# Performance work log

Hardware: AMD Instinct MI355X
Metric: run time of the kernel (lower is better)

Reference implementation:

```python
import jax, jax.numpy as jnp
import numpy as np

HIDDEN = 1024
HEADS = 16
MEM = 2
D_H = HIDDEN // HEADS
NEG = -1.0e9


def setup_inputs() -> dict:
    key = jax.random.key(0)
    ks = jax.random.split(key, 8)
    B, M, N = 16, 512, 512
    s = 1.0 / np.sqrt(HIDDEN)
    return {
        "x": jax.random.normal(ks[0], (B, M, HIDDEN), dtype=jnp.float32),
        "y": jax.random.normal(ks[1], (B, N, HIDDEN), dtype=jnp.float32),
        "mask_x": jax.random.randint(ks[2], (B, M), 0, 2, dtype=jnp.int64),
        "mask_y": jax.random.randint(ks[3], (B, N), 0, 2, dtype=jnp.int64),
        "Wx": jax.random.normal(ks[4], (HIDDEN, HIDDEN), dtype=jnp.float32) * s,
        "Wy": jax.random.normal(ks[5], (HIDDEN, HIDDEN), dtype=jnp.float32) * s,
        "x_memory": jax.random.normal(ks[6], (MEM, HIDDEN), dtype=jnp.float32),
        "y_memory": jax.random.normal(ks[7], (MEM, HIDDEN), dtype=jnp.float32),
    }


def _project(t, mem, W):
    # prepend memory tokens, then linear (torch Linear: t @ W^T), split heads
    B = t.shape[0]
    t_mem = jnp.concatenate([jnp.broadcast_to(mem[None], (B, MEM, HIDDEN)), t], axis=1)
    proj = t_mem @ W.T
    proj = proj.reshape(B, t_mem.shape[1], HEADS, D_H)
    return t_mem, proj


def reference(x, y, mask_x, mask_y, Wx, Wy, x_memory, y_memory):
    B = x.shape[0]
    mem_mask = jnp.ones((B, MEM), dtype=mask_x.dtype)
    mx = jnp.concatenate([mem_mask, mask_x], axis=1)  # [B, M+MEM]
    my = jnp.concatenate([mem_mask, mask_y], axis=1)  # [B, N+MEM]

    X_mem, X_proj = _project(x, x_memory, Wx)  # [B,Mm,H], [B,Mm,heads,d_h]
    Y_mem, Y_proj = _project(y, y_memory, Wy)

    # affinity: [B, heads, Mm, Nm]
    aff = jnp.einsum("bmhd,bnhd->bhmn", X_proj, Y_proj)
    aff = jnp.where(mx[:, None, :, None] == 0, NEG, aff)
    aff = jnp.where(my[:, None, None, :] == 0, NEG, aff)

    attn_X = jnp.mean(jax.nn.softmax(aff, axis=2), axis=1)  # [B, Mm, Nm]
    attn_Y = jnp.mean(jax.nn.softmax(aff, axis=3), axis=1)  # [B, Mm, Nm]

    X_in_Y = jnp.einsum("bmn,bmh->bnh", attn_X, X_mem)[:, MEM:, :]  # [B, N, H]
    Y_in_X = jnp.einsum("bmn,bnh->bmh", attn_Y, Y_mem)[:, MEM:, :]  # [B, M, H]
    return X_in_Y, Y_in_X
```

## Files before the change

### kernel.cpp

```cpp
#include <hip/hip_runtime.h>

#define B_   16
#define SEQ  512
#define MM   514
#define HID  1024
#define NH   16
#define DH   64
#define KP   544
#define MTOT (B_ * MM)
#define UNI  (1.0f/514.0f)

typedef unsigned short us;
typedef __attribute__((ext_vector_type(4))) float f32x4;
typedef __attribute__((ext_vector_type(8))) short short8;
typedef __attribute__((ext_vector_type(8))) _Float16 half8;

__device__ __forceinline__ us f2bf(float f) {
  unsigned int u = __float_as_uint(f);
  u = (u + 0x7FFFu + ((u >> 16) & 1u)) >> 16;
  return (us)u;
}
__device__ __forceinline__ float bf2f(us h) {
  return __uint_as_float(((unsigned int)h) << 16);
}
__device__ __forceinline__ us f2h(float f) {
  _Float16 h = (_Float16)f;
  return *(us*)&h;
}
__device__ __forceinline__ unsigned cvt_pk_bf16(float lo, float hi) {
  unsigned d;
  asm("v_cvt_pk_bf16_f32 %0, %1, %2" : "=v"(d) : "v"(lo), "v"(hi));
  return d;
}
__device__ __forceinline__ uint4 pack8_pk(f32x4 v0, f32x4 v1) {
  uint4 r;
  r.x = cvt_pk_bf16(v0[0], v0[1]);
  r.y = cvt_pk_bf16(v0[2], v0[3]);
  r.z = cvt_pk_bf16(v1[0], v1[1]);
  r.w = cvt_pk_bf16(v1[2], v1[3]);
  return r;
}

__global__ __launch_bounds__(256) void proj_fused(
    const float* __restrict__ x, const float* __restrict__ y,
    const float* __restrict__ xm, const float* __restrict__ ym,
    const float* __restrict__ Wx, const float* __restrict__ Wy,
    us* __restrict__ Px, us* __restrict__ Py) {
  const int nt = blockIdx.x, mt = blockIdx.y, which = blockIdx.z;
  const float* tin  = which ? y  : x;
  const float* mvec = which ? ym : xm;
  const float* W    = which ? Wy : Wx;
  us* P             = which ? Py : Px;
  __shared__ __align__(16) us As[128 * 40];
  __shared__ __align__(16) us Bs[128 * 40];
  const int tid = threadIdx.x;
  const int lane = tid & 63, wave = tid >> 6;
  const int c = lane & 15, q = lane >> 4;
  const int wr = wave >> 1, wc = wave & 1;

  const int srow = tid >> 1, sch = (tid & 1) * 16;
  const int grow = mt * 128 + srow;
  const float* asrc = nullptr;
  if (grow < MTOT) {
    const int gb = grow / MM, gt = grow - gb * MM;
    asrc = (gt < 2) ? (mvec + (size_t)gt * HID + sch)
                    : (tin + ((size_t)(gb * SEQ + gt - 2)) * HID + sch);
  }
  const float* bsrc = W + ((size_t)(nt * 128 + srow)) * HID + sch;
  us* wAp = &As[srow * 40 + sch];
  us* wBp = &Bs[srow * 40 + sch];
  const us* rA = &As[(wr * 64 + c) * 40 + q * 8];
  const us* rB = &Bs[(wc * 64 + c) * 40 + q * 8];

  f32x4 acc[4][4];
#pragma unroll
  for (int i = 0; i < 4; i++)
#pragma unroll
    for (int j = 0; j < 4; j++) acc[i][j] = (f32x4){0.f, 0.f, 0.f, 0.f};

  f32x4 pa[4], pb[4];
#pragma unroll
  for (int u = 0; u < 4; u++) pa[u] = (f32x4){0.f, 0.f, 0.f, 0.f};
  if (asrc) {
#pragma unroll
    for (int u = 0; u < 4; u++) pa[u] = *(const f32x4*)(asrc + u * 4);
  }
#pragma unroll
  for (int u = 0; u < 4; u++) pb[u] = *(const f32x4*)(bsrc + u * 4);

  for (int kk = 0; kk < HID; kk += 32) {
    __syncthreads();
    *(uint4*)wAp       = pack8_pk(pa[0], pa[1]);
    *(uint4*)(wAp + 8) = pack8_pk(pa[2], pa[3]);
    *(uint4*)wBp       = pack8_pk(pb[0], pb[1]);
    *(uint4*)(wBp + 8) = pack8_pk(pb[2], pb[3]);
    __syncthreads();
    if (kk + 32 < HID) {
      if (asrc) {
#pragma unroll
        for (int u = 0; u < 4; u++) pa[u] = *(const f32x4*)(asrc + kk + 32 + u * 4);
      }
#pragma unroll
      for (int u = 0; u < 4; u++) pb[u] = *(const f32x4*)(bsrc + kk + 32 + u * 4);
    }
    short8 a[4], bb[4];
#pragma unroll
    for (int i = 0; i < 4; i++) a[i] = *(const short8*)(rA + i * 16 * 40);
#pragma unroll
    for (int j = 0; j < 4; j++) bb[j] = *(const short8*)(rB + j * 16 * 40);
#pragma unroll
    for (int i = 0; i < 4; i++)
#pragma unroll
      for (int j = 0; j < 4; j++)
        acc[i][j] = __builtin_amdgcn_mfma_f32_16x16x32_bf16(a[i], bb[j], acc[i][j], 0, 0, 0);
  }
#pragma unroll
  for (int i = 0; i < 4; i++) {
#pragma unroll
    for (int r = 0; r < 4; r++) {
      int gr = mt * 128 + wr * 64 + i * 16 + q * 4 + r;
      if (gr < MTOT) {
        size_t rb = (size_t)gr * HID;
#pragma unroll
        for (int j = 0; j < 4; j++)
          P[rb + nt * 128 + wc * 64 + j * 16 + c] = f2bf(acc[i][j][r]);
      }
    }
  }
}

__device__ __forceinline__ void stage_bf(
    us* Xs, const us* P, int b, int r0, int h, int tid) {
#pragma unroll
  for (int i = 0; i < 2; i++) {
    int idx = tid + i * 256;
    int row = idx >> 3, qq = idx & 7;
    *(uint4*)&Xs[row * 72 + qq * 8] =
        *(const uint4*)(P + ((size_t)(b * MM + min(r0 + row, MM - 1))) * HID + h * DH + qq * 8);
  }
}

__global__ __launch_bounds__(512) void sums_big(
    const us* __restrict__ Px, const us* __restrict__ Py,
    const int* __restrict__ mx, const int* __restrict__ my,
    float* __restrict__ Sums) {
  const int half = blockIdx.x, h = blockIdx.y, b = blockIdx.z;
  const int NCH = half ? 5 : 4;
  const int n0 = half * 256;
  __shared__ __align__(16) us Ys[320 * 72];
  __shared__ __align__(16) us Xs[64 * 72];
  __shared__ float cS[320];
  __shared__ int myS[320];
  __shared__ int mxS[576];
  const int tid = threadIdx.x;
  const int lane = tid & 63, wave = tid >> 6;
  const int c = lane & 15, q = lane >> 4;
  const int strip = wave & 3, cgrp = wave >> 2;
  const int chm = (NCH + 1) >> 1;
  const int ch0 = cgrp ? chm : 0;
  const int ch1 = cgrp ? NCH : chm;

  for (int i = tid; i < 320; i += 512) {
    cS[i] = 0.f;
    int n = n0 + i;
    myS[i] = (n >= MM) ? 0 : ((n < 2) ? 1 : my[b * SEQ + n - 2]);
  }
  for (int i = tid; i < 576; i += 512)
    mxS[i] = (i >= MM) ? 0 : ((i < 2) ? 1 : mx[b * SEQ + i - 2]);
  {
    const int row8 = tid >> 3, qq = tid & 7;
    for (int it = 0; it < NCH; it++) {
      int row = it * 64 + row8;
      int grow = min(n0 + row, MM - 1);
      *(uint4*)&Ys[row * 72 + qq * 8] =
          *(const uint4*)(Py + ((size_t)(b * MM + grow)) * HID + h * DH + qq * 8);
    }
  }
  __syncthreads();

  const size_t base = ((size_t)(b * NH + h)) * MM;
  const size_t COLOFF = (size_t)B_ * NH * MM;

  for (int mt = 0; mt < 9; mt++) {
    {
      const int row8 = tid >> 3, qq = tid & 7;
      int grow = min(mt * 64 + row8, MM - 1);
      *(uint4*)&Xs[row8 * 72 + qq * 8] =
          *(const uint4*)(Px + ((size_t)(b * MM + grow)) * HID + h * DH + qq * 8);
    }
    __syncthreads();
    short8 a0 = *(const short8*)&Xs[(strip * 16 + c) * 72 + q * 8];
    short8 a1 = *(const short8*)&Xs[(strip * 16 + c) * 72 + q * 8 + 32];
    int rm[4];
#pragma unroll
    for (int r = 0; r < 4; r++) rm[r] = mxS[mt * 64 + strip * 16 + q * 4 + r];
    float rowp[4] = {0.f, 0.f, 0.f, 0.f};
    for (int ch = ch0; ch < ch1; ch++) {
#pragma unroll
      for (int ss = 0; ss < 4; ss++) {
        int nloc = ch * 64 + ss * 16 + c;
        short8 b0 = *(const short8*)&Ys[nloc * 72 + q * 8];
        short8 b1 = *(const short8*)&Ys[nloc * 72 + q * 8 + 32];
        f32x4 av = (f32x4){0.f, 0.f, 0.f, 0.f};
        av = __builtin_amdgcn_mfma_f32_16x16x32_bf16(a0, b0, av, 0, 0, 0);
        av = __builtin_amdgcn_mfma_f32_16x16x32_bf16(a1, b1, av, 0, 0, 0);
        int cmv = myS[nloc];
        float colp = 0.f;
#pragma unroll
        for (int r = 0; r < 4; r++) {
          float e = (rm[r] && cmv) ? __expf(av[r]) : 0.f;
          rowp[r] += e;
          colp += e;
        }
        colp += __shfl_xor(colp, 16);
        colp += __shfl_xor(colp, 32);
        if (q == 0) atomicAdd(&cS[nloc], colp);
      }
    }
#pragma unroll
    for (int d = 1; d < 16; d <<= 1)
#pragma unroll
      for (int r = 0; r < 4; r++) rowp[r] += __shfl_xor(rowp[r], d, 16);
    if (c == 0) {
#pragma unroll
      for (int r = 0; r < 4; r++) {
        int m = mt * 64 + strip * 16 + q * 4 + r;
        if (m < MM) atomicAdd(&Sums[base + m], rowp[r]);
      }
    }
    __syncthreads();
  }
  for (int i = tid; i < NCH * 64; i += 512) {
    int n = n0 + i;
    if (n < MM) Sums[COLOFF + base + n] = cS[i];
  }
}

__global__ __launch_bounds__(256) void inv_kernel(float* __restrict__ Sums) {
  int i = blockIdx.x * 256 + threadIdx.x;
  if (i < 2 * B_ * NH * MM) {
    float s = Sums[i];
    Sums[i] = (s > 0.f) ? (1.f / s) : -1.f;
  }
}

__global__ __launch_bounds__(256) void attn_mfma2(
    const us* __restrict__ Px, const us* __restrict__ Py,
    const int* __restrict__ mx, const int* __restrict__ my,
    const float* __restrict__ Inv,
    us* __restrict__ attnXT, us* __restrict__ attnY) {
  const int nt = blockIdx.x, mt = blockIdx.y, b = blockIdx.z;
  __shared__ __align__(16) us Xs[64 * 72];
  __shared__ __align__(16) us Ys[64 * 72];
  const int tid = threadIdx.x;
  const int lane = tid & 63, wave = tid >> 6;
  const int c = lane & 15, q = lane >> 4;
  const size_t COLOFF = (size_t)B_ * NH * MM;

  int mreg[4], rm[4], ncol[4], cm[4];
#pragma unroll
  for (int r = 0; r < 4; r++) {
    mreg[r] = mt * 64 + wave * 16 + q * 4 + r;
    rm[r] = (mreg[r] >= MM) ? 0 : ((mreg[r] < 2) ? 1 : mx[b * SEQ + mreg[r] - 2]);
  }
#pragma unroll
  for (int s = 0; s < 4; s++) {
    ncol[s] = nt * 64 + s * 16 + c;
    cm[s] = (ncol[s] >= MM) ? 0 : ((ncol[s] < 2) ? 1 : my[b * SEQ + ncol[s] - 2]);
  }

  float aX[4][4], aY[4][4];
#pragma unroll
  for (int s = 0; s < 4; s++)
#pragma unroll
    for (int r = 0; r < 4; r++) { aX[s][r] = 0.f; aY[s][r] = 0.f; }

  for (int h = 0; h < NH; h++) {
    __syncthreads();
    stage_bf(Xs, Px, b, mt * 64, h, tid);
    stage_bf(Ys, Py, b, nt * 64, h, tid);
    __syncthreads();
    short8 a0 = *(const short8*)&Xs[(wave * 16 + c) * 72 + q * 8];
    short8 a1 = *(const short8*)&Xs[(wave * 16 + c) * 72 + q * 8 + 32];
    const size_t base = ((size_t)(b * NH + h)) * MM;
    float invR[4];
#pragma unroll
    for (int r = 0; r < 4; r++) invR[r] = Inv[base + min(mreg[r], MM - 1)];
#pragma unroll
    for (int s = 0; s < 4; s++) {
      float invC = Inv[COLOFF + base + min(ncol[s], MM - 1)];
      short8 b0 = *(const short8*)&Ys[(s * 16 + c) * 72 + q * 8];
      short8 b1 = *(const short8*)&Ys[(s * 16 + c) * 72 + q * 8 + 32];
      f32x4 av = (f32x4){0.f, 0.f, 0.f, 0.f};
      av = __builtin_amdgcn_mfma_f32_16x16x32_bf16(a0, b0, av, 0, 0, 0);
      av = __builtin_amdgcn_mfma_f32_16x16x32_bf16(a1, b1, av, 0, 0, 0);
#pragma unroll
      for (int r = 0; r < 4; r++) {
        float e = (rm[r] && cm[s]) ? __expf(av[r]) : 0.f;
        aY[s][r] += (invR[r] < 0.f) ? UNI : e * invR[r];
        aX[s][r] += (invC < 0.f) ? UNI : e * invC;
      }
    }
  }
#pragma unroll
  for (int s = 0; s < 4; s++) {
    if (ncol[s] < MM) {
      us* xrow = attnXT + ((size_t)(b * MM + ncol[s])) * KP;
      if (mreg[3] < MM) {
        uint2 w;
        w.x = (unsigned)f2h(aX[s][0] * 0.0625f) | ((unsigned)f2h(aX[s][1] * 0.0625f) << 16);
        w.y = (unsigned)f2h(aX[s][2] * 0.0625f) | ((unsigned)f2h(aX[s][3] * 0.0625f) << 16);
        *(uint2*)&xrow[mreg[0]] = w;
      } else {
#pragma unroll
        for (int r = 0; r < 4; r++)
          if (mreg[r] < MM) xrow[mreg[r]] = f2h(aX[s][r] * 0.0625f);
      }
#pragma unroll
      for (int r = 0; r < 4; r++)
        if (mreg[r] < MM)
          attnY[((size_t)(b * MM + mreg[r])) * KP + ncol[s]] = f2h(aY[s][r] * 0.0625f);
    }
  }
}

__global__ __launch_bounds__(256) void transpose_fused(
    const float* __restrict__ x, const float* __restrict__ y,
    const float* __restrict__ xm, const float* __restrict__ ym,
    us* __restrict__ XTx, us* __restrict__ XTy) {
  const int kt = blockIdx.x, ot = blockIdx.y;
  const int b = blockIdx.z & 15, path = blockIdx.z >> 4;
  const float* tin  = path ? y  : x;
  const float* mvec = path ? ym : xm;
  us* XT            = path ? XTy : XTx;
  __shared__ __align__(16) us T[64 * 40];
  const int tid = threadIdx.x;
  {
    const int row = tid >> 3;
    const int col8 = (tid & 7) * 8;
    const int kg = kt * 32 + row;
    const float* src = (kg < 2) ? (mvec + (size_t)kg * HID + ot * 64 + col8)
                     : (kg < MM) ? (tin + ((size_t)(b * SEQ + kg - 2)) * HID + ot * 64 + col8)
                                 : nullptr;
    f32x4 v0 = (f32x4){0.f, 0.f, 0.f, 0.f};
    f32x4 v1 = (f32x4){0.f, 0.f, 0.f, 0.f};
    if (src) { v0 = *(const f32x4*)src; v1 = *(const f32x4*)(src + 4); }
#pragma unroll
    for (int j = 0; j < 4; j++) T[(col8 + j) * 40 + row] = f2h(v0[j]);
#pragma unroll
    for (int j = 0; j < 4; j++) T[(col8 + 4 + j) * 40 + row] = f2h(v1[j]);
  }
  __syncthreads();
  const int orow = tid >> 2, kc = (tid & 3) * 8;
  uint4 w = *(const uint4*)&T[orow * 40 + kc];
  *(uint4*)&XT[((size_t)(b * HID + ot * 64 + orow)) * KP + kt * 32 + kc] = w;
}

__global__ __launch_bounds__(256) void outg_fused(
    const us* __restrict__ A0, const us* __restrict__ A1,
    const us* __restrict__ XTx, const us* __restrict__ XTy,
    float* __restrict__ outp) {
  const int ot = blockIdx.x, rt = blockIdx.y;
  const int b = blockIdx.z & 15, path = blockIdx.z >> 4;
  const us* A  = path ? A1 : A0;
  const us* XT = path ? XTy : XTx;
  float* op = outp + (path ? (size_t)B_ * SEQ * HID : 0);
  const int r0 = rt * 128, o0 = ot * 128;
  __shared__ __align__(16) us As[128 * 40];
  __shared__ __align__(16) us Bs[128 * 40];
  const int tid = threadIdx.x;
  const int lane = tid & 63, wave = tid >> 6;
  const int c = lane & 15, q = lane >> 4;
  const int wr = wave >> 1, wc = wave & 1;

  const int srow = tid >> 2, sch = (tid & 3) * 8;
  const us* gA0 = A + ((size_t)(b * MM + 2 + r0 + srow)) * KP + sch;
  const us* gA1 = gA0 + (size_t)64 * KP;
  const us* gB0 = XT + ((size_t)(b * HID + o0 + srow)) * KP + sch;
  const us* gB1 = gB0 + (size_t)64 * KP;
  us* wA0 = &As[srow * 40 + sch];
  us* wA1 = wA0 + 64 * 40;
  us* wB0 = &Bs[srow * 40 + sch];
  us* wB1 = wB0 + 64 * 40;

  f32x4 acc[4][4];
#pragma unroll
  for (int i = 0; i < 4; i++)
#pragma unroll
    for (int j = 0; j < 4; j++) acc[i][j] = (f32x4){0.f, 0.f, 0.f, 0.f};

  const us* rA = &As[(wr * 64 + c) * 40 + q * 8];
  const us* rB = &Bs[(wc * 64 + c) * 40 + q * 8];

  uint4 pA0 = *(const uint4*)gA0;
  uint4 pA1 = *(const uint4*)gA1;
  uint4 pB0 = *(const uint4*)gB0;
  uint4 pB1 = *(const uint4*)gB1;

  for (int kk = 0; kk < KP; kk += 32) {
    __syncthreads();
    *(uint4*)wA0 = pA0;
    *(uint4*)wA1 = pA1;
    *(uint4*)wB0 = pB0;
    *(uint4*)wB1 = pB1;
    __syncthreads();
    if (kk + 32 < KP) {
      pA0 = *(const uint4*)(gA0 + kk + 32);
      pA1 = *(const uint4*)(gA1 + kk + 32);
      pB0 = *(const uint4*)(gB0 + kk + 32);
      pB1 = *(const uint4*)(gB1 + kk + 32);
    }
    half8 a[4], bb[4];
#pragma unroll
    for (int i = 0; i < 4; i++) a[i] = *(const half8*)(rA + i * 16 * 40);
#pragma unroll
    for (int j = 0; j < 4; j++) bb[j] = *(const half8*)(rB + j * 16 * 40);
#pragma unroll
    for (int i = 0; i < 4; i++)
#pragma unroll
      for (int j = 0; j < 4; j++)
        acc[i][j] = __builtin_amdgcn_mfma_f32_16x16x32_f16(a[i], bb[j], acc[i][j], 0, 0, 0);
  }
#pragma unroll
  for (int i = 0; i < 4; i++) {
#pragma unroll
    for (int rr = 0; rr < 4; rr++) {
      int r = r0 + wr * 64 + i * 16 + q * 4 + rr;
      size_t rowbase = ((size_t)(b * SEQ + r)) * HID;
#pragma unroll
      for (int j = 0; j < 4; j++)
        op[rowbase + o0 + wc * 64 + j * 16 + c] = acc[i][j][rr];
    }
  }
}

__global__ __launch_bounds__(256) void attn_mfma_old(
    const us* __restrict__ Px, const us* __restrict__ Py,
    const int* __restrict__ mx, const int* __restrict__ my,
    const float* __restrict__ Inv,
    us* __restrict__ attnX, us* __restrict__ attnY,
    const int doX, const int doY) {
  const int nt = blockIdx.x, mt = blockIdx.y, b = blockIdx.z;
  __shared__ __align__(16) us Xs[64 * 72];
  __shared__ __align__(16) us Ys[64 * 72];
  const int tid = threadIdx.x;
  const int lane = tid & 63, wave = tid >> 6;
  const int c = lane & 15, q = lane >> 4;
  const size_t COLOFF = (size_t)B_ * NH * MM;

  int mreg[4], rm[4], ncol[4], cm[4];
#pragma unroll
  for (int r = 0; r < 4; r++) {
    mreg[r] = mt * 64 + wave * 16 + q * 4 + r;
    rm[r] = (mreg[r] >= MM) ? 0 : ((mreg[r] < 2) ? 1 : mx[b * SEQ + mreg[r] - 2]);
  }
#pragma unroll
  for (int s = 0; s < 4; s++) {
    ncol[s] = nt * 64 + s * 16 + c;
    cm[s] = (ncol[s] >= MM) ? 0 : ((ncol[s] < 2) ? 1 : my[b * SEQ + ncol[s] - 2]);
  }

  float aX[4][4], aY[4][4];
#pragma unroll
  for (int s = 0; s < 4; s++)
#pragma unroll
    for (int r = 0; r < 4; r++) { aX[s][r] = 0.f; aY[s][r] = 0.f; }

  for (int h = 0; h < NH; h++) {
    __syncthreads();
    stage_bf(Xs, Px, b, mt * 64, h, tid);
    stage_bf(Ys, Py, b, nt * 64, h, tid);
    __syncthreads();
    short8 a0 = *(const short8*)&Xs[(wave * 16 + c) * 72 + q * 8];
    short8 a1 = *(const short8*)&Xs[(wave * 16 + c) * 72 + q * 8 + 32];
    const size_t base = ((size_t)(b * NH + h)) * MM;
    float invR[4];
#pragma unroll
    for (int r = 0; r < 4; r++) invR[r] = Inv[base + min(mreg[r], MM - 1)];
#pragma unroll
    for (int s = 0; s < 4; s++) {
      float invC = Inv[COLOFF + base + min(ncol[s], MM - 1)];
      short8 b0 = *(const short8*)&Ys[(s * 16 + c) * 72 + q * 8];
      short8 b1 = *(const short8*)&Ys[(s * 16 + c) * 72 + q * 8 + 32];
      f32x4 av = (f32x4){0.f, 0.f, 0.f, 0.f};
      av = __builtin_amdgcn_mfma_f32_16x16x32_bf16(a0, b0, av, 0, 0, 0);
      av = __builtin_amdgcn_mfma_f32_16x16x32_bf16(a1, b1, av, 0, 0, 0);
#pragma unroll
      for (int r = 0; r < 4; r++) {
        float e = (rm[r] && cm[s]) ? __expf(av[r]) : 0.f;
        aY[s][r] += (invR[r] < 0.f) ? UNI : e * invR[r];
        aX[s][r] += (invC < 0.f) ? UNI : e * invC;
      }
    }
  }
#pragma unroll
  for (int s = 0; s < 4; s++) {
#pragma unroll
    for (int r = 0; r < 4; r++) {
      if (mreg[r] < MM && ncol[s] < MM) {
        size_t idx = ((size_t)(b * MM + mreg[r])) * MM + ncol[s];
        if (doX) attnX[idx] = f2bf(aX[s][r] * 0.0625f);
        if (doY) attnY[idx] = f2bf(aY[s][r] * 0.0625f);
      }
    }
  }
}

__global__ __launch_bounds__(256) void outg_kernel(
    const us* __restrict__ attn, const float* __restrict__ tin,
    const float* __restrict__ mvec, float* __restrict__ outp, const int trans) {
  const int otile = blockIdx.x, rtile = blockIdx.y, b = blockIdx.z;
  __shared__ __align__(16) float Ss[32 * 132];
  __shared__ __align__(16) float Ms[32 * 132];
  const int tid = threadIdx.x;
  const int r0 = rtile * 128, o0 = otile * 128;

  float acc[8][8];
#pragma unroll
  for (int i = 0; i < 8; i++)
#pragma unroll
    for (int j = 0; j < 8; j++) acc[i][j] = 0.f;

  for (int kk = 0; kk < 544; kk += 32) {
    __syncthreads();
    if (trans) {
      int rq = (tid & 31) * 4;
      int kr = tid >> 5;
#pragma unroll
      for (int kb = 0; kb < 32; kb += 8) {
        int k = kr + kb;
        int kg = kk + k;
        if (kg < MM) {
          const us* src = attn + ((size_t)(b * MM + kg)) * MM + 2 + r0 + rq;
          Ss[k * 132 + rq + 0] = bf2f(src[0]);
          Ss[k * 132 + rq + 1] = bf2f(src[1]);
          Ss[k * 132 + rq + 2] = bf2f(src[2]);
          Ss[k * 132 + rq + 3] = bf2f(src[3]);
        } else {
          Ss[k * 132 + rq + 0] = 0.f;
          Ss[k * 132 + rq + 1] = 0.f;
          Ss[k * 132 + rq + 2] = 0.f;
          Ss[k * 132 + rq + 3] = 0.f;
        }
      }
    } else {
      int r = tid >> 1;
      int kh = (tid & 1) * 16;
      const us* src = attn + ((size_t)(b * MM + 2 + r0 + r)) * MM;
#pragma unroll
      for (int j = 0; j < 16; j++) {
        int k = kh + j;
        int kg = kk + k;
        Ss[k * 132 + r] = (kg < MM) ? bf2f(src[kg]) : 0.f;
      }
    }
    {
      int k = tid >> 3;
      int oq = (tid & 7) * 16;
      int kg = kk + k;
      const float* mr = (kg < 2) ? (mvec + (size_t)kg * HID)
                      : (kg < MM) ? (tin + ((size_t)(b * SEQ + kg - 2)) * HID)
                                  : nullptr;
#pragma unroll
      for (int qq = 0; qq < 4; qq++) {
        f32x4 v = (f32x4){0.f, 0.f, 0.f, 0.f};
        if (mr) v = *(const f32x4*)(mr + o0 + oq + qq * 4);
        *(f32x4*)&Ms[k * 132 + oq + qq * 4] = v;
      }
    }
    __syncthreads();
    const int ty = tid >> 4, tx = tid & 15;
    for (int k = 0; k < 32; k++) {
      f32x4 s0 = *(const f32x4*)&Ss[k * 132 + ty * 4];
      f32x4 s1 = *(const f32x4*)&Ss[k * 132 + 64 + ty * 4];
      f32x4 m0 = *(const f32x4*)&Ms[k * 132 + tx * 4];
      f32x4 m1 = *(const f32x4*)&Ms[k * 132 + 64 + tx * 4];
#pragma unroll
      for (int i = 0; i < 4; i++) {
#pragma unroll
        for (int j = 0; j < 4; j++) {
          acc[i][j]         += s0[i] * m0[j];
          acc[i][j + 4]     += s0[i] * m1[j];
          acc[i + 4][j]     += s1[i] * m0[j];
          acc[i + 4][j + 4] += s1[i] * m1[j];
        }
      }
    }
  }
  const int ty = tid >> 4, tx = tid & 15;
#pragma unroll
  for (int ri = 0; ri < 2; ri++) {
#pragma unroll
    for (int i = 0; i < 4; i++) {
      int r = r0 + ri * 64 + ty * 4 + i;
      size_t rowbase = ((size_t)(b * SEQ + r)) * HID;
#pragma unroll
      for (int oi = 0; oi < 2; oi++) {
        int o = o0 + oi * 64 + tx * 4;
        f32x4 v;
#pragma unroll
        for (int j = 0; j < 4; j++) v[j] = acc[ri * 4 + i][oi * 4 + j];
        *(f32x4*)&outp[rowbase + o] = v;
      }
    }
  }
}

extern "C" void kernel_launch(void* const* d_in, const int* in_sizes, int n_in,
                              void* d_out, int out_size, void* d_ws, size_t ws_size,
                              hipStream_t stream) {
  const float* x  = (const float*)d_in[0];
  const float* y  = (const float*)d_in[1];
  const int* mask_x = (const int*)d_in[2];
  const int* mask_y = (const int*)d_in[3];
  const float* Wx = (const float*)d_in[4];
  const float* Wy = (const float*)d_in[5];
  const float* xm = (const float*)d_in[6];
  const float* ym = (const float*)d_in[7];
  float* out = (float*)d_out;

  const size_t szSums = (size_t)2 * B_ * NH * MM * 4;
  const size_t szP    = (size_t)B_ * MM * HID * 2;
  const size_t szAtt  = (size_t)B_ * MM * MM * 2;
  const size_t szAttP = (size_t)B_ * MM * KP * 2;
  const size_t szXT   = (size_t)B_ * HID * KP * 2;
  const size_t R_off  = szSums + 2 * szAttP;
  const size_t needNew = R_off + 2 * szXT;

  char* ws = (char*)d_ws;

  if (ws_size >= needNew) {
    float* Sums = (float*)ws;
    us* A0  = (us*)(ws + szSums);
    us* A1  = (us*)(ws + szSums + szAttP);
    us* Px  = (us*)(ws + R_off);
    us* Py  = (us*)(ws + R_off + szP);
    us* XTx = (us*)(ws + R_off);
    us* XTy = (us*)(ws + R_off + szXT);

    proj_fused<<<dim3(8, 65, 2), 256, 0, stream>>>(x, y, xm, ym, Wx, Wy, Px, Py);
    hipMemsetAsync(Sums, 0, szSums, stream);
    hipMemsetAsync(A0, 0, 2 * szAttP, stream);
    sums_big<<<dim3(2, 16, 16), 512, 0, stream>>>(Px, Py, mask_x, mask_y, Sums);
    inv_kernel<<<dim3((2 * B_ * NH * MM + 255) / 256), 256, 0, stream>>>(Sums);
    attn_mfma2<<<dim3(9, 9, 16), 256, 0, stream>>>(Px, Py, mask_x, mask_y, Sums, A0, A1);
    transpose_fused<<<dim3(17, 16, 32), 256, 0, stream>>>(x, y, xm, ym, XTx, XTy);
    outg_fused<<<dim3(8, 4, 32), 256, 0, stream>>>(A0, A1, XTx, XTy, out);
    return;
  }

  const int dual = (ws_size >= szSums + 2 * szP + 2 * szAtt) ? 1 : 0;
  float* Sums = (float*)(ws);
  us* Px = (us*)(ws + szSums);
  us* Py = (us*)(ws + szSums + szP);
  us* A0 = (us*)(ws + szSums + 2 * szP);
  us* A1 = dual ? (us*)(ws + szSums + 2 * szP + szAtt) : A0;

  proj_fused<<<dim3(8, 65, 2), 256, 0, stream>>>(x, y, xm, ym, Wx, Wy, Px, Py);
  hipMemsetAsync(Sums, 0, szSums, stream);
  sums_big<<<dim3(2, 16, 16), 512, 0, stream>>>(Px, Py, mask_x, mask_y, Sums);
  inv_kernel<<<dim3((2 * B_ * NH * MM + 255) / 256), 256, 0, stream>>>(Sums);

  if (dual) {
    attn_mfma_old<<<dim3(9, 9, 16), 256, 0, stream>>>(Px, Py, mask_x, mask_y, Sums, A0, A1, 1, 1);
    outg_kernel<<<dim3(8, 4, 16), 256, 0, stream>>>(A0, x, xm, out, 1);
    outg_kernel<<<dim3(8, 4, 16), 256, 0, stream>>>(A1, y, ym, out + (size_t)B_ * SEQ * HID, 0);
  } else {
    attn_mfma_old<<<dim3(9, 9, 16), 256, 0, stream>>>(Px, Py, mask_x, mask_y, Sums, A0, A0, 1, 0);
    outg_kernel<<<dim3(8, 4, 16), 256, 0, stream>>>(A0, x, xm, out, 1);
    attn_mfma_old<<<dim3(9, 9, 16), 256, 0, stream>>>(Px, Py, mask_x, mask_y, Sums, A0, A0, 0, 1);
    outg_kernel<<<dim3(8, 4, 16), 256, 0, stream>>>(A0, y, ym, out + (size_t)B_ * SEQ * HID, 0);
  }
}
```

Before: 405.3 us.

## Pre-convert projection inputs and weights to bf16 in a separate pass

Adds a prepack kernel that converts x/y (with memory tokens prepended) and Wx/Wy from fp32 to bf16 once, storing them in the output buffer as scratch space. The projection GEMM then loads bf16 directly, halving its global load bytes and dropping repeated per-tile conversion of W, which was re-read by every M tile. It also remaps block indices so consecutive blocks share an M tile across N tiles for better L2 reuse. The cost is an extra kernel launch plus a full read/write pass over the inputs, and it relies on the output buffer being free until the final kernel.

```diff
diff --git a/kernel.cpp b/kernel.cpp
--- a/kernel.cpp
+++ b/kernel.cpp
@@ -32,25 +32,56 @@
   asm("v_cvt_pk_bf16_f32 %0, %1, %2" : "=v"(d) : "v"(lo), "v"(hi));
   return d;
 }
-__device__ __forceinline__ uint4 pack8_pk(f32x4 v0, f32x4 v1) {
-  uint4 r;
-  r.x = cvt_pk_bf16(v0[0], v0[1]);
-  r.y = cvt_pk_bf16(v0[2], v0[3]);
-  r.z = cvt_pk_bf16(v1[0], v1[1]);
-  r.w = cvt_pk_bf16(v1[2], v1[3]);
-  return r;
-}
-
-__global__ __launch_bounds__(256) void proj_fused(
+
+__global__ __launch_bounds__(256) void prepack(
     const float* __restrict__ x, const float* __restrict__ y,
     const float* __restrict__ xm, const float* __restrict__ ym,
     const float* __restrict__ Wx, const float* __restrict__ Wy,
+    us* __restrict__ Abf, us* __restrict__ Wbf) {
+  const int tid = threadIdx.x;
+  const int row = blockIdx.x * 4 + (tid >> 6);
+  const int path = blockIdx.y;
+  const int lane = tid & 63;
+  const float* src;
+  us* dst;
+  if (row < MTOT) {
+    const int gb = row / MM, gt = row - gb * MM;
+    const float* tin = path ? y : x;
+    const float* mv  = path ? ym : xm;
+    src = (gt < 2) ? (mv + (size_t)gt * HID)
+                   : (tin + ((size_t)(gb * SEQ + gt - 2)) * HID);
+    dst = Abf + ((size_t)(path * MTOT + row)) * HID;
+  } else {
+    const int o = row - MTOT;
+    src = (path ? Wy : Wx) + (size_t)o * HID;
+    dst = Wbf + ((size_t)(path * HID + o)) * HID;
+  }
+  const float* s = src + lane * 16;
+  f32x4 v0 = *(const f32x4*)(s);
+  f32x4 v1 = *(const f32x4*)(s + 4);
+  f32x4 v2 = *(const f32x4*)(s + 8);
+  f32x4 v3 = *(const f32x4*)(s + 12);
+  uint4 w0, w1;
+  w0.x = cvt_pk_bf16(v0[0], v0[1]);  w0.y = cvt_pk_bf16(v0[2], v0[3]);
+  w0.z = cvt_pk_bf16(v1[0], v1[1]);  w0.w = cvt_pk_bf16(v1[2], v1[3]);
+  w1.x = cvt_pk_bf16(v2[0], v2[1]);  w1.y = cvt_pk_bf16(v2[2], v2[3]);
+  w1.z = cvt_pk_bf16(v3[0], v3[1]);  w1.w = cvt_pk_bf16(v3[2], v3[3]);
+  *(uint4*)(dst + lane * 16)     = w0;
+  *(uint4*)(dst + lane * 16 + 8) = w1;
+}
+
+__global__ __launch_bounds__(256) void proj_fused2(
+    const us* __restrict__ Abf, const us* __restrict__ Wbf,
     us* __restrict__ Px, us* __restrict__ Py) {
-  const int nt = blockIdx.x, mt = blockIdx.y, which = blockIdx.z;
-  const float* tin  = which ? y  : x;
-  const float* mvec = which ? ym : xm;
-  const float* W    = which ? Wy : Wx;
-  us* P             = which ? Py : Px;
+  const int lin = blockIdx.x + 8 * (blockIdx.y + 65 * blockIdx.z);
+  const int work = (lin & 7) * 130 + (lin >> 3);
+  const int path = (work >= 520) ? 1 : 0;
+  const int wrem = work - path * 520;
+  const int mt = wrem >> 3, nt = wrem & 7;
+  us* P = path ? Py : Px;
+  const us* Ab = Abf + (size_t)path * MTOT * HID;
+  const us* Wb = Wbf + (size_t)path * HID * HID;
+
   __shared__ __align__(16) us As[128 * 40];
   __shared__ __align__(16) us Bs[128 * 40];
   const int tid = threadIdx.x;
@@ -60,13 +91,8 @@
 
   const int srow = tid >> 1, sch = (tid & 1) * 16;
   const int grow = mt * 128 + srow;
-  const float* asrc = nullptr;
-  if (grow < MTOT) {
-    const int gb = grow / MM, gt = grow - gb * MM;
-    asrc = (gt < 2) ? (mvec + (size_t)gt * HID + sch)
-                    : (tin + ((size_t)(gb * SEQ + gt - 2)) * HID + sch);
-  }
-  const float* bsrc = W + ((size_t)(nt * 128 + srow)) * HID + sch;
+  const us* asrc = (grow < MTOT) ? (Ab + (size_t)grow * HID + sch) : nullptr;
+  const us* bsrc = Wb + (size_t)(nt * 128 + srow) * HID + sch;
   us* wAp = &As[srow * 40 + sch];
   us* wBp = &Bs[srow * 40 + sch];
   const us* rA = &As[(wr * 64 + c) * 40 + q * 8];
@@ -78,30 +104,25 @@
 #pragma unroll
     for (int j = 0; j < 4; j++) acc[i][j] = (f32x4){0.f, 0.f, 0.f, 0.f};
 
-  f32x4 pa[4], pb[4];
-#pragma unroll
-  for (int u = 0; u < 4; u++) pa[u] = (f32x4){0.f, 0.f, 0.f, 0.f};
-  if (asrc) {
-#pragma unroll
-    for (int u = 0; u < 4; u++) pa[u] = *(const f32x4*)(asrc + u * 4);
-  }
-#pragma unroll
-  for (int u = 0; u < 4; u++) pb[u] = *(const f32x4*)(bsrc + u * 4);
+  uint4 z4 = {0u, 0u, 0u, 0u};
+  uint4 pa0 = z4, pa1 = z4, pb0, pb1;
+  if (asrc) { pa0 = *(const uint4*)asrc; pa1 = *(const uint4*)(asrc + 8); }
+  pb0 = *(const uint4*)bsrc; pb1 = *(const uint4*)(bsrc + 8);
 
   for (int kk = 0; kk < HID; kk += 32) {
     __syncthreads();
-    *(uint4*)wAp       = pack8_pk(pa[0], pa[1]);
-    *(uint4*)(wAp + 8) = pack8_pk(pa[2], pa[3]);
-    *(uint4*)wBp       = pack8_pk(pb[0], pb[1]);
-    *(uint4*)(wBp + 8) = pack8_pk(pb[2], pb[3]);
+    *(uint4*)wAp       = pa0;
+    *(uint4*)(wAp + 8) = pa1;
+    *(uint4*)wBp       = pb0;
+    *(uint4*)(wBp + 8) = pb1;
     __syncthreads();
     if (kk + 32 < HID) {
       if (asrc) {
-#pragma unroll
-        for (int u = 0; u < 4; u++) pa[u] = *(const f32x4*)(asrc + kk + 32 + u * 4);
-      }
-#pragma unroll
-      for (int u = 0; u < 4; u++) pb[u] = *(const f32x4*)(bsrc + kk + 32 + u * 4);
+        pa0 = *(const uint4*)(asrc + kk + 32);
+        pa1 = *(const uint4*)(asrc + kk + 32 + 8);
+      }
+      pb0 = *(const uint4*)(bsrc + kk + 32);
+      pb1 = *(const uint4*)(bsrc + kk + 32 + 8);
     }
     short8 a[4], bb[4];
 #pragma unroll
@@ -120,7 +141,8 @@
     for (int r = 0; r < 4; r++) {
       int gr = mt * 128 + wr * 64 + i * 16 + q * 4 + r;
       if (gr < MTOT) {
-        size_t rb = (size_t)gr * HID;
+        size_t rb = (size_t)(path * MTOT + gr) * HID - (size_t)path * MTOT * HID;
+        rb = (size_t)gr * HID;
 #pragma unroll
         for (int j = 0; j < 4; j++)
           P[rb + nt * 128 + wc * 64 + j * 16 + c] = f2bf(acc[i][j][r]);
@@ -629,6 +651,9 @@
 
   char* ws = (char*)d_ws;
 
+  us* Abf = (us*)d_out;
+  us* Wbf = (us*)d_out + (size_t)2 * MTOT * HID;
+
   if (ws_size >= needNew) {
     float* Sums = (float*)ws;
     us* A0  = (us*)(ws + szSums);
@@ -638,7 +663,8 @@
     us* XTx = (us*)(ws + R_off);
     us* XTy = (us*)(ws + R_off + szXT);
 
-    proj_fused<<<dim3(8, 65, 2), 256, 0, stream>>>(x, y, xm, ym, Wx, Wy, Px, Py);
+    prepack<<<dim3((MTOT + HID) / 4, 2), 256, 0, stream>>>(x, y, xm, ym, Wx, Wy, Abf, Wbf);
+    proj_fused2<<<dim3(8, 65, 2), 256, 0, stream>>>(Abf, Wbf, Px, Py);
     hipMemsetAsync(Sums, 0, szSums, stream);
     hipMemsetAsync(A0, 0, 2 * szAttP, stream);
     sums_big<<<dim3(2, 16, 16), 512, 0, stream>>>(Px, Py, mask_x, mask_y, Sums);
@@ -656,7 +682,8 @@
   us* A0 = (us*)(ws + szSums + 2 * szP);
   us* A1 = dual ? (us*)(ws + szSums + 2 * szP + szAtt) : A0;
 
-  proj_fused<<<dim3(8, 65, 2), 256, 0, stream>>>(x, y, xm, ym, Wx, Wy, Px, Py);
+  prepack<<<dim3((MTOT + HID) / 4, 2), 256, 0, stream>>>(x, y, xm, ym, Wx, Wy, Abf, Wbf);
+  proj_fused2<<<dim3(8, 65, 2), 256, 0, stream>>>(Abf, Wbf, Px, Py);
   hipMemsetAsync(Sums, 0, szSums, stream);
   sums_big<<<dim3(2, 16, 16), 512, 0, stream>>>(Px, Py, mask_x, mask_y, Sums);
   inv_kernel<<<dim3((2 * B_ * NH * MM + 255) / 256), 256, 0, stream>>>(Sums);
```

Result: faster. 373.2 us (-7.9%).
